# Optimization experiments

Measured on AMD Instinct MI355X. Metric: run time of the kernel, lower is better.

Reference implementation:

```python
import jax, jax.numpy as jnp
import numpy as np


def setup_inputs() -> dict:
    key = jax.random.key(0)
    ks = jax.random.split(key, 4)
    B, S, D, F, E = 2, 2048, 1024, 2048, 8
    x = jax.random.normal(ks[0], (B, S, D), dtype=jnp.float32)
    router_w = jax.random.normal(ks[1], (D, E), dtype=jnp.float32) * 0.02
    w_in = jax.random.normal(ks[2], (E, D, 2 * F), dtype=jnp.float32) * 0.02
    w_out = jax.random.normal(ks[3], (E, F, D), dtype=jnp.float32) * 0.02
    out_bias = jnp.zeros((D,), dtype=jnp.float32)
    return {"x": x, "router_w": router_w, "w_in": w_in, "w_out": w_out,
            "out_bias": out_bias, "top_k": 2}


def reference(x, router_w, w_in, w_out, out_bias, top_k):
    B, S, D = x.shape
    E = router_w.shape[1]
    xt = x.reshape(-1, D)                      # [T, D]
    T = xt.shape[0]

    # --- top-k router (JetMoeTopKGating) ---
    logits = xt @ router_w                     # [T, E]
    top_vals, top_idx = jax.lax.top_k(logits, top_k)   # [T, k]
    gates = jax.nn.softmax(top_vals, axis=-1)          # [T, k], softmax over selected
    # dense combine weights [T, E]: gate where selected, 0 elsewhere
    combine = jnp.zeros((T, E), dtype=x.dtype).at[
        jnp.arange(T)[:, None], top_idx].add(gates)

    # --- grouped expert MLP (GLU: silu(h1) * h2) ---
    out = jnp.zeros((T, D), dtype=x.dtype)
    for e in range(E):                         # E is small & static
        h = xt @ w_in[e]                       # [T, 2F]
        g, v = jnp.split(h, 2, axis=-1)
        y = (jax.nn.silu(g) * v) @ w_out[e]    # [T, D]
        out = out + combine[:, e:e + 1] * y
    out = out.reshape(B, S, D) + out_bias

    # --- load-balancing aux loss ---
    probs = jax.nn.softmax(logits, axis=-1)    # [T, E]
    # fraction of routed assignments per expert
    sel = jax.nn.one_hot(top_idx, E, dtype=x.dtype).sum(axis=1)  # [T, E]
    f = sel.mean(axis=0) / top_k               # [E]
    P = probs.mean(axis=0)                     # [E]
    aux_loss = E * jnp.sum(f * P)
    return out, aux_loss
```

## Files before the change

### kernel.cpp

```cpp
#include <hip/hip_runtime.h>


#define T_TOK 4096
#define DIM   1024
#define NEXP  8
#define FF    2048
#define YB    24
#define BK    64

typedef __attribute__((ext_vector_type(8))) short short8;
typedef __attribute__((ext_vector_type(4))) float f32x4;

__device__ __forceinline__ unsigned short f2b(float f) {
  unsigned int u = __builtin_bit_cast(unsigned int, f);
  u += 0x7fffu + ((u >> 16) & 1u);
  return (unsigned short)(u >> 16);
}

__device__ __forceinline__ void gll16(const unsigned short* g, unsigned short* l) {
  __builtin_amdgcn_global_load_lds(
      (const __attribute__((address_space(1))) unsigned int*)g,
      (__attribute__((address_space(3))) unsigned int*)l, 16, 0, 0);
}

__device__ __forceinline__ void stage_tile(const unsigned short* __restrict__ gbase,
                                           size_t ldk, int k0,
                                           unsigned short* __restrict__ lds,
                                           int w, int lane) {
#pragma unroll
  for (int i = 0; i < 4; i++) {
    const int s = w * 256 + i * 64 + lane;
    const int r = s >> 3;
    const int pc = s & 7;
    const int gc = ((pc - r) & 7) * 8;
    gll16(gbase + (size_t)r * ldk + k0 + gc, lds + (size_t)s * 8);
  }
}

__device__ __forceinline__ short8 frag_read(const unsigned short* __restrict__ lds,
                                            int row, int kk, int quad) {
  const int p = ((kk * 4 + quad) + row) & 7;
  return __builtin_bit_cast(short8, *(const uint4*)(lds + (size_t)row * BK + p * 8));
}

__global__ void router_k(const float* __restrict__ x, const float* __restrict__ rw,
                         int* __restrict__ tok_e, float* __restrict__ tok_g,
                         float* __restrict__ psum_part) {
  const int t = blockIdx.x * 4 + (threadIdx.x >> 6);
  const int lane = threadIdx.x & 63;
  double acc[8];
#pragma unroll
  for (int e = 0; e < 8; e++) acc[e] = 0.0;
  const float* xr = x + (size_t)t * DIM;
#pragma unroll
  for (int d0 = 0; d0 < DIM; d0 += 256) {
    const int d = d0 + lane * 4;
    float4 xv = *(const float4*)(xr + d);
    const float* rwr = rw + d * 8;
#pragma unroll
    for (int j = 0; j < 4; j++) {
      double xd = (double)((j == 0) ? xv.x : (j == 1) ? xv.y : (j == 2) ? xv.z : xv.w);
#pragma unroll
      for (int e = 0; e < 8; e++) acc[e] += xd * (double)rwr[j * 8 + e];
    }
  }
#pragma unroll
  for (int off = 32; off > 0; off >>= 1) {
#pragma unroll
    for (int e = 0; e < 8; e++) acc[e] += __shfl_down(acc[e], off, 64);
  }
  __shared__ float pblk[8];
  if (threadIdx.x < 8) pblk[threadIdx.x] = 0.f;
  __syncthreads();
  if (lane == 0) {
    int i0 = -1, i1 = -1;
    double v0 = -1e300, v1 = -1e300;
#pragma unroll
    for (int e = 0; e < 8; e++) {
      double v = acc[e];
      if (v > v0) { v1 = v0; i1 = i0; v0 = v; i0 = e; }
      else if (v > v1) { v1 = v; i1 = e; }
    }
    float g1 = 1.f / (1.f + __expf((float)(v0 - v1)));
    tok_e[t * 2] = i0; tok_e[t * 2 + 1] = i1;
    tok_g[t * 2] = 1.f - g1; tok_g[t * 2 + 1] = g1;
    float s = 0.f; float p[8];
#pragma unroll
    for (int e = 0; e < 8; e++) { p[e] = __expf((float)(acc[e] - v0)); s += p[e]; }
    float inv = 1.f / s;
#pragma unroll
    for (int e = 0; e < 8; e++) atomicAdd(&pblk[e], p[e] * inv);
  }
  __syncthreads();
  if (threadIdx.x < 8) psum_part[blockIdx.x * 8 + threadIdx.x] = pblk[threadIdx.x];
}

__global__ __launch_bounds__(1024) void bucket_k(
    const int* __restrict__ tok_e, const float* __restrict__ tok_g,
    const float* __restrict__ psum_part,
    int* __restrict__ cnt, int* __restrict__ off,
    int* __restrict__ slot_t, float* __restrict__ slot_g,
    float* __restrict__ out_aux) {
  const int tid = threadIdx.x;
  const int lane = tid & 63;
  __shared__ int lcnt[8];
  __shared__ float fsum[8];
  if (tid < 8) { lcnt[tid] = 0; fsum[tid] = 0.f; }
  __syncthreads();
#pragma unroll
  for (int rep = 0; rep < 4; rep++) {
    const int t = rep * 1024 + tid;
    const int e0 = tok_e[t * 2], e1 = tok_e[t * 2 + 1];
    const float g0 = tok_g[t * 2], g1 = tok_g[t * 2 + 1];
#pragma unroll
    for (int which = 0; which < 2; which++) {
      const int e = which ? e1 : e0;
      const float g = which ? g1 : g0;
      int slot = 0;
#pragma unroll
      for (int ex = 0; ex < 8; ex++) {
        unsigned long long m = __ballot(e == ex);
        int base = 0;
        int first = __ffsll((long long)m) - 1;
        if (m != 0ull && lane == first) base = atomicAdd(&lcnt[ex], __popcll(m));
        base = __shfl(base, first & 63, 64);
        if (e == ex) slot = base + __popcll(m & ((1ull << lane) - 1ull));
      }
      slot_t[e * T_TOK + slot] = t;
      slot_g[e * T_TOK + slot] = g;
    }
  }
  float p[8];
#pragma unroll
  for (int e = 0; e < 8; e++) p[e] = psum_part[tid * 8 + e];
#pragma unroll
  for (int o = 32; o > 0; o >>= 1) {
#pragma unroll
    for (int e = 0; e < 8; e++) p[e] += __shfl_down(p[e], o, 64);
  }
  if (lane == 0) {
#pragma unroll
    for (int e = 0; e < 8; e++) atomicAdd(&fsum[e], p[e]);
  }
  __syncthreads();
  if (tid == 0) {
    int o = 0; float aux = 0.f;
    for (int e = 0; e < 8; e++) {
      cnt[e] = lcnt[e]; off[e] = o; o += lcnt[e];
      aux += ((float)lcnt[e] / (4096.f * 2.f)) * (fsum[e] / 4096.f);
    }
    out_aux[0] = 8.f * aux;
  }
}

__global__ void init_out_k(float* __restrict__ out, const float* __restrict__ bias) {
  int i = blockIdx.x * 256 + threadIdx.x;
  out[i] = bias[i & (DIM - 1)];
}

__global__ void transpose_k(const float* __restrict__ src, unsigned short* __restrict__ dst,
                            int K, int N) {
  __shared__ float tile[64][65];
  const int e = blockIdx.z;
  const int kb = blockIdx.y * 64, nb = blockIdx.x * 64;
  const float* s = src + (size_t)e * K * N;
  unsigned short* d = dst + (size_t)e * N * K;
  const int tid = threadIdx.x;
  const int r = tid >> 2;
  const int cseg = (tid & 3) * 16;
#pragma unroll
  for (int j = 0; j < 16; j += 4) {
    float4 v = *(const float4*)(s + (size_t)(kb + r) * N + nb + cseg + j);
    tile[r][cseg + j] = v.x; tile[r][cseg + j + 1] = v.y;
    tile[r][cseg + j + 2] = v.z; tile[r][cseg + j + 3] = v.w;
  }
  __syncthreads();
#pragma unroll
  for (int j = 0; j < 16; j += 4) {
    ushort4 o4;
    o4.x = f2b(tile[cseg + j][r]);
    o4.y = f2b(tile[cseg + j + 1][r]);
    o4.z = f2b(tile[cseg + j + 2][r]);
    o4.w = f2b(tile[cseg + j + 3][r]);
    *(ushort4*)(d + (size_t)(nb + r) * K + kb + cseg + j) = o4;
  }
}

__global__ void gather_k(const float* __restrict__ x, const int* __restrict__ cnt,
                         const int* __restrict__ off, const int* __restrict__ slot_t,
                         unsigned short* __restrict__ A1) {
  const int e = blockIdx.z;
  const int rb = blockIdx.y * 128;
  const int c = cnt[e];
  if (rb >= c) return;
  const int o = off[e];
  const int cb = blockIdx.x * 128;
  for (int i = threadIdx.x; i < 128 * 32; i += 256) {
    int r = i >> 5;
    int seg = cb + (i & 31) * 4;
    int row = rb + r;
    if (row >= c) continue;
    int t = slot_t[e * T_TOK + row];
    float4 v = *(const float4*)(x + (size_t)t * DIM + seg);
    ushort4 o4;
    o4.x = f2b(v.x); o4.y = f2b(v.y); o4.z = f2b(v.z); o4.w = f2b(v.w);
    *(ushort4*)(A1 + (size_t)(o + row) * DIM + seg) = o4;
  }
}

__global__ __launch_bounds__(256, 2) void gemm1_k(
    const unsigned short* __restrict__ A1, const unsigned short* __restrict__ W1T,
    unsigned short* __restrict__ H, const int* __restrict__ cnt, const int* __restrict__ off) {
  const int e = blockIdx.z;
  const int c = cnt[e];
  const int rb = blockIdx.y * 128;
  if (rb >= c) return;
  const int o = off[e];
  const unsigned short* Ab = A1 + (size_t)(o + rb) * DIM;
  const unsigned short* Bgb = W1T + ((size_t)e * 4096 + blockIdx.x * 128) * DIM;
  const unsigned short* Bvb = Bgb + (size_t)2048 * DIM;

  __shared__ __align__(16) unsigned short As[128][BK];
  __shared__ __align__(16) unsigned short Bg[128][BK];
  __shared__ __align__(16) unsigned short Bv[128][BK];

  const int tid = threadIdx.x;
  const int lane = tid & 63;
  const int w = tid >> 6;
  const int mq = (w >> 1) * 64;
  const int nq = (w & 1) * 64;
  const int fr = lane & 15;
  const int quad = lane >> 4;

  f32x4 accg[4][4], accv[4][4];
  const f32x4 zero = {0.f, 0.f, 0.f, 0.f};
#pragma unroll
  for (int i = 0; i < 4; i++)
#pragma unroll
    for (int j = 0; j < 4; j++) { accg[i][j] = zero; accv[i][j] = zero; }

  for (int k0 = 0; k0 < DIM; k0 += BK) {
    stage_tile(Ab,  DIM, k0, &As[0][0], w, lane);
    stage_tile(Bgb, DIM, k0, &Bg[0][0], w, lane);
    stage_tile(Bvb, DIM, k0, &Bv[0][0], w, lane);
    __syncthreads();

#pragma unroll
    for (int kk = 0; kk < 2; kk++) {
      short8 af[4], bgf[4], bvf[4];
#pragma unroll
      for (int mi = 0; mi < 4; mi++)
        af[mi] = frag_read(&As[0][0], mq + mi * 16 + fr, kk, quad);
#pragma unroll
      for (int ni = 0; ni < 4; ni++) {
        bgf[ni] = frag_read(&Bg[0][0], nq + ni * 16 + fr, kk, quad);
        bvf[ni] = frag_read(&Bv[0][0], nq + ni * 16 + fr, kk, quad);
      }
#pragma unroll
      for (int mi = 0; mi < 4; mi++)
#pragma unroll
        for (int ni = 0; ni < 4; ni++) {
          accg[mi][ni] = __builtin_amdgcn_mfma_f32_16x16x32_bf16(af[mi], bgf[ni], accg[mi][ni], 0, 0, 0);
          accv[mi][ni] = __builtin_amdgcn_mfma_f32_16x16x32_bf16(af[mi], bvf[ni], accv[mi][ni], 0, 0, 0);
        }
    }
    __syncthreads();
  }

  const int vrows = c - rb;
  const int cb = blockIdx.x * 128;
#pragma unroll
  for (int mi = 0; mi < 4; mi++) {
#pragma unroll
    for (int ni = 0; ni < 4; ni++) {
      const int col = nq + ni * 16 + fr;
      const int rowb = mq + mi * 16 + quad * 4;
#pragma unroll
      for (int r = 0; r < 4; r++) {
        const int row = rowb + r;
        if (row < vrows) {
          float g = accg[mi][ni][r];
          float v = accv[mi][ni][r];
          float s = g / (1.f + __expf(-g)) * v;
          H[(size_t)(o + rb + row) * FF + cb + col] = f2b(s);
        }
      }
    }
  }
}

__global__ __launch_bounds__(256, 2) void gemm2_k(
    const unsigned short* __restrict__ H, const unsigned short* __restrict__ W2T,
    float* __restrict__ out, const int* __restrict__ cnt, const int* __restrict__ off,
    const int* __restrict__ slot_t, const float* __restrict__ slot_g) {
  const int e = blockIdx.z;
  const int c = cnt[e];
  const int rb = blockIdx.y * 128;
  if (rb >= c) return;
  const int o = off[e];
  const unsigned short* Ab = H + (size_t)(o + rb) * FF;
  const unsigned short* Bb = W2T + ((size_t)e * 1024 + blockIdx.x * 128) * FF;

  __shared__ __align__(16) unsigned short As[128][BK];
  __shared__ __align__(16) unsigned short Bs[128][BK];

  const int tid = threadIdx.x;
  const int lane = tid & 63;
  const int w = tid >> 6;
  const int mq = (w >> 1) * 64;
  const int nq = (w & 1) * 64;
  const int fr = lane & 15;
  const int quad = lane >> 4;

  f32x4 acc[4][4];
  const f32x4 zero = {0.f, 0.f, 0.f, 0.f};
#pragma unroll
  for (int i = 0; i < 4; i++)
#pragma unroll
    for (int j = 0; j < 4; j++) acc[i][j] = zero;

  for (int k0 = 0; k0 < FF; k0 += BK) {
    stage_tile(Ab, FF, k0, &As[0][0], w, lane);
    stage_tile(Bb, FF, k0, &Bs[0][0], w, lane);
    __syncthreads();

#pragma unroll
    for (int kk = 0; kk < 2; kk++) {
      short8 af[4], bf[4];
#pragma unroll
      for (int mi = 0; mi < 4; mi++)
        af[mi] = frag_read(&As[0][0], mq + mi * 16 + fr, kk, quad);
#pragma unroll
      for (int ni = 0; ni < 4; ni++)
        bf[ni] = frag_read(&Bs[0][0], nq + ni * 16 + fr, kk, quad);
#pragma unroll
      for (int mi = 0; mi < 4; mi++)
#pragma unroll
        for (int ni = 0; ni < 4; ni++)
          acc[mi][ni] = __builtin_amdgcn_mfma_f32_16x16x32_bf16(af[mi], bf[ni], acc[mi][ni], 0, 0, 0);
    }
    __syncthreads();
  }

  const int vrows = c - rb;
  const int cb = blockIdx.x * 128;
#pragma unroll
  for (int mi = 0; mi < 4; mi++) {
    const int rowb = mq + mi * 16 + quad * 4;
#pragma unroll
    for (int r = 0; r < 4; r++) {
      const int row = rowb + r;
      if (row < vrows) {
        const int t = slot_t[e * T_TOK + rb + row];
        const float gt = slot_g[e * T_TOK + rb + row];
        float* orow = out + (size_t)t * DIM + cb;
#pragma unroll
        for (int ni = 0; ni < 4; ni++) {
          const int col = nq + ni * 16 + fr;
          atomicAdd(orow + col, gt * acc[mi][ni][r]);
        }
      }
    }
  }
}

extern "C" void kernel_launch(void* const* d_in, const int* in_sizes, int n_in,
                              void* d_out, int out_size, void* d_ws, size_t ws_size,
                              hipStream_t stream) {
  const float* x     = (const float*)d_in[0];
  const float* rw    = (const float*)d_in[1];
  const float* w_in  = (const float*)d_in[2];
  const float* w_out = (const float*)d_in[3];
  const float* bias  = (const float*)d_in[4];
  float* out = (float*)d_out;

  char* ws = (char*)d_ws;
  int*   cnt    = (int*)ws;
  int*   off    = (int*)(ws + 32);
  int*   slot_t = (int*)(ws + 256);
  float* slot_g = (float*)(ws + 256 + 131072);
  int*   tok_e  = (int*)(ws + (512 << 10));
  float* tok_g  = (float*)(ws + (576 << 10));
  float* psum_p = (float*)(ws + (640 << 10));
  unsigned short* A1  = (unsigned short*)(ws + ((size_t)1 << 20));
  unsigned short* H   = (unsigned short*)(ws + ((size_t)18 << 20));
  unsigned short* W1T = (unsigned short*)(ws + ((size_t)51 << 20));
  unsigned short* W2T = (unsigned short*)(ws + ((size_t)116 << 20));

  init_out_k<<<16384, 256, 0, stream>>>(out, bias);
  transpose_k<<<dim3(64, 16, 8), 256, 0, stream>>>(w_in, W1T, 1024, 4096);
  transpose_k<<<dim3(16, 32, 8), 256, 0, stream>>>(w_out, W2T, 2048, 1024);
  router_k<<<1024, 256, 0, stream>>>(x, rw, tok_e, tok_g, psum_p);
  bucket_k<<<1, 1024, 0, stream>>>(tok_e, tok_g, psum_p, cnt, off,
                                   slot_t, slot_g, out + (size_t)T_TOK * DIM);
  gather_k<<<dim3(8, YB, 8), 256, 0, stream>>>(x, cnt, off, slot_t, A1);
  gemm1_k<<<dim3(16, YB, 8), 256, 0, stream>>>(A1, W1T, H, cnt, off);
  gemm2_k<<<dim3(8, YB, 8), 256, 0, stream>>>(H, W2T, out, cnt, off, slot_t, slot_g);
}
```

Measured before the change: 481.3 us.

## Replace atomic scatter in expert GEMM2 with dense store plus combine kernel

gemm2 now writes unweighted expert outputs densely into a per-slot buffer instead of doing gated atomicAdds into the output, and a new combine kernel gathers the two expert rows per token, applies gates and bias, and writes the output once. This removes the bias-init kernel and fp32 atomic traffic, at the cost of an extra 32MB write/read round trip. The bucket kernel now records each token's slot instead of per-slot gates. YB drops from 24 to 16, which caps each expert at 2048 rows; that is enough for typical routing but would drop rows if an expert got more tokens. The Y buffer reuses the W1T workspace region after gemm1 finishes.

Result: faster. 468.8 us (-2.6%).

```diff
diff --git a/kernel.cpp b/kernel.cpp
--- a/kernel.cpp
+++ b/kernel.cpp
@@ -5,7 +5,7 @@
 #define DIM   1024
 #define NEXP  8
 #define FF    2048
-#define YB    24
+#define YB    16
 #define BK    64
 
 typedef __attribute__((ext_vector_type(8))) short short8;
@@ -99,7 +99,7 @@
     const int* __restrict__ tok_e, const float* __restrict__ tok_g,
     const float* __restrict__ psum_part,
     int* __restrict__ cnt, int* __restrict__ off,
-    int* __restrict__ slot_t, float* __restrict__ slot_g,
+    int* __restrict__ slot_t, int* __restrict__ tok_s,
     float* __restrict__ out_aux) {
   const int tid = threadIdx.x;
   const int lane = tid & 63;
@@ -111,11 +111,9 @@
   for (int rep = 0; rep < 4; rep++) {
     const int t = rep * 1024 + tid;
     const int e0 = tok_e[t * 2], e1 = tok_e[t * 2 + 1];
-    const float g0 = tok_g[t * 2], g1 = tok_g[t * 2 + 1];
 #pragma unroll
     for (int which = 0; which < 2; which++) {
       const int e = which ? e1 : e0;
-      const float g = which ? g1 : g0;
       int slot = 0;
 #pragma unroll
       for (int ex = 0; ex < 8; ex++) {
@@ -127,7 +125,7 @@
         if (e == ex) slot = base + __popcll(m & ((1ull << lane) - 1ull));
       }
       slot_t[e * T_TOK + slot] = t;
-      slot_g[e * T_TOK + slot] = g;
+      tok_s[t * 2 + which] = slot;
     }
   }
   float p[8];
@@ -151,11 +149,6 @@
     }
     out_aux[0] = 8.f * aux;
   }
-}
-
-__global__ void init_out_k(float* __restrict__ out, const float* __restrict__ bias) {
-  int i = blockIdx.x * 256 + threadIdx.x;
-  out[i] = bias[i & (DIM - 1)];
 }
 
 __global__ void transpose_k(const float* __restrict__ src, unsigned short* __restrict__ dst,
@@ -291,8 +284,7 @@
 
 __global__ __launch_bounds__(256, 2) void gemm2_k(
     const unsigned short* __restrict__ H, const unsigned short* __restrict__ W2T,
-    float* __restrict__ out, const int* __restrict__ cnt, const int* __restrict__ off,
-    const int* __restrict__ slot_t, const float* __restrict__ slot_g) {
+    float* __restrict__ Y, const int* __restrict__ cnt, const int* __restrict__ off) {
   const int e = blockIdx.z;
   const int c = cnt[e];
   const int rb = blockIdx.y * 128;
@@ -351,17 +343,36 @@
     for (int r = 0; r < 4; r++) {
       const int row = rowb + r;
       if (row < vrows) {
-        const int t = slot_t[e * T_TOK + rb + row];
-        const float gt = slot_g[e * T_TOK + rb + row];
-        float* orow = out + (size_t)t * DIM + cb;
+        float* yrow = Y + (size_t)(o + rb + row) * DIM + cb;
 #pragma unroll
         for (int ni = 0; ni < 4; ni++) {
           const int col = nq + ni * 16 + fr;
-          atomicAdd(orow + col, gt * acc[mi][ni][r]);
+          yrow[col] = acc[mi][ni][r];
         }
       }
     }
   }
+}
+
+__global__ void combine_k(const float* __restrict__ Y, const int* __restrict__ tok_e,
+                          const int* __restrict__ tok_s, const float* __restrict__ tok_g,
+                          const int* __restrict__ off, const float* __restrict__ bias,
+                          float* __restrict__ out) {
+  const int t = blockIdx.x;
+  const int d = threadIdx.x * 4;
+  const int e0 = tok_e[t * 2], e1 = tok_e[t * 2 + 1];
+  const int gs0 = off[e0] + tok_s[t * 2];
+  const int gs1 = off[e1] + tok_s[t * 2 + 1];
+  const float g0 = tok_g[t * 2], g1 = tok_g[t * 2 + 1];
+  float4 y0 = *(const float4*)(Y + (size_t)gs0 * DIM + d);
+  float4 y1 = *(const float4*)(Y + (size_t)gs1 * DIM + d);
+  float4 b = *(const float4*)(bias + d);
+  float4 r;
+  r.x = b.x + g0 * y0.x + g1 * y1.x;
+  r.y = b.y + g0 * y0.y + g1 * y1.y;
+  r.z = b.z + g0 * y0.z + g1 * y1.z;
+  r.w = b.w + g0 * y0.w + g1 * y1.w;
+  *(float4*)(out + (size_t)t * DIM + d) = r;
 }
 
 extern "C" void kernel_launch(void* const* d_in, const int* in_sizes, int n_in,
@@ -378,22 +389,23 @@
   int*   cnt    = (int*)ws;
   int*   off    = (int*)(ws + 32);
   int*   slot_t = (int*)(ws + 256);
-  float* slot_g = (float*)(ws + 256 + 131072);
+  int*   tok_s  = (int*)(ws + 256 + 131072);
   int*   tok_e  = (int*)(ws + (512 << 10));
   float* tok_g  = (float*)(ws + (576 << 10));
   float* psum_p = (float*)(ws + (640 << 10));
   unsigned short* A1  = (unsigned short*)(ws + ((size_t)1 << 20));
   unsigned short* H   = (unsigned short*)(ws + ((size_t)18 << 20));
   unsigned short* W1T = (unsigned short*)(ws + ((size_t)51 << 20));
+  float*          Yb  = (float*)(ws + ((size_t)51 << 20));
   unsigned short* W2T = (unsigned short*)(ws + ((size_t)116 << 20));
 
-  init_out_k<<<16384, 256, 0, stream>>>(out, bias);
   transpose_k<<<dim3(64, 16, 8), 256, 0, stream>>>(w_in, W1T, 1024, 4096);
   transpose_k<<<dim3(16, 32, 8), 256, 0, stream>>>(w_out, W2T, 2048, 1024);
   router_k<<<1024, 256, 0, stream>>>(x, rw, tok_e, tok_g, psum_p);
   bucket_k<<<1, 1024, 0, stream>>>(tok_e, tok_g, psum_p, cnt, off,
-                                   slot_t, slot_g, out + (size_t)T_TOK * DIM);
+                                   slot_t, tok_s, out + (size_t)T_TOK * DIM);
   gather_k<<<dim3(8, YB, 8), 256, 0, stream>>>(x, cnt, off, slot_t, A1);
   gemm1_k<<<dim3(16, YB, 8), 256, 0, stream>>>(A1, W1T, H, cnt, off);
-  gemm2_k<<<dim3(8, YB, 8), 256, 0, stream>>>(H, W2T, out, cnt, off, slot_t, slot_g);
-}
+  gemm2_k<<<dim3(8, YB, 8), 256, 0, stream>>>(H, W2T, Yb, cnt, off);
+  combine_k<<<T_TOK, 256, 0, stream>>>(Yb, tok_e, tok_s, tok_g, off, bias, out);
+}
```
